# Optimization experiments

Hardware: AMD Instinct MI355X
Metric: run time of the kernel (lower is better)

Reference implementation:

```python
import jax, jax.numpy as jnp
import numpy as np

PRE_NMS_THRESH = 0.05
PRE_NMS_TOP_N = 1000
NMS_THRESH = 0.6
FPN_POST_NMS_TOP_N = 100
MIN_SIZE = 0.0
NUM_CLASSES = 80
BBOX_W = (10.0, 10.0, 5.0, 5.0)
SCALE_CLAMP = float(np.log(1000.0 / 16.0))
CLASS_OFFSET = 2000.0  # > max image coordinate after clipping
N_IMG = 16
LEVELS = [(100, 152, 8, 64), (50, 76, 16, 128), (25, 38, 32, 256), (13, 19, 64, 512), (7, 10, 128, 1024)]


def _make_anchors(H, W, stride, size):
    cx = np.arange(W, dtype=np.float32) * stride
    cy = np.arange(H, dtype=np.float32) * stride
    xx, yy = np.meshgrid(cx, cy)
    ctr = np.stack([xx, yy, xx, yy], -1).reshape(-1, 4)
    base = np.array([-size / 2.0, -size / 2.0, size / 2.0, size / 2.0], np.float32)
    return jnp.asarray((ctr + base).astype(np.float32))


def setup_inputs() -> dict:
    key = jax.random.key(0)
    ks = jax.random.split(key, 10)
    inp = {}
    for i, (H, W, st, sz) in enumerate(LEVELS):
        inp[f"cls{i}"] = jax.random.normal(ks[i], (N_IMG, NUM_CLASSES, H, W), jnp.float32) * 2.0 - 4.0
        inp[f"reg{i}"] = jax.random.normal(ks[5 + i], (N_IMG, 4, H, W), jnp.float32)
        inp[f"anc{i}"] = _make_anchors(H, W, st, sz)
    inp["image_sizes"] = jnp.tile(jnp.array([[800, 1216]], jnp.int32), (N_IMG, 1))
    return inp


def _decode(deltas, anchors):
    wx, wy, ww, wh = BBOX_W
    w = anchors[..., 2] - anchors[..., 0] + 1.0
    h = anchors[..., 3] - anchors[..., 1] + 1.0
    cx = anchors[..., 0] + 0.5 * w
    cy = anchors[..., 1] + 0.5 * h
    dx = deltas[..., 0] / wx
    dy = deltas[..., 1] / wy
    dw = jnp.minimum(deltas[..., 2] / ww, SCALE_CLAMP)
    dh = jnp.minimum(deltas[..., 3] / wh, SCALE_CLAMP)
    pcx = dx * w + cx
    pcy = dy * h + cy
    pw = jnp.exp(dw) * w
    ph = jnp.exp(dh) * h
    return jnp.stack([pcx - 0.5 * (pw - 1.0), pcy - 0.5 * (ph - 1.0),
                      pcx + 0.5 * (pw - 1.0), pcy + 0.5 * (ph - 1.0)], -1)


def _level(cls, reg, anc):
    n, C, H, W = cls.shape  # A = 1
    scores = jax.nn.sigmoid(jnp.transpose(cls, (0, 2, 3, 1)).reshape(n, -1, C))  # [n, HW, C]
    regf = jnp.transpose(reg, (0, 2, 3, 1)).reshape(n, -1, 4)  # [n, HW, 4]
    flat = scores.reshape(n, -1)
    masked = jnp.where(flat > PRE_NMS_THRESH, flat, 0.0)
    vals, idx = jax.lax.top_k(masked, PRE_NMS_TOP_N)  # emulates thresh + per-image clamp
    loc = idx // C
    cl = idx % C
    deltas = jnp.take_along_axis(regf, loc[..., None], axis=1)  # [n, K, 4]
    boxes = _decode(deltas, anc[loc])
    valid = vals > PRE_NMS_THRESH
    sc = jnp.where(valid, jnp.sqrt(jnp.maximum(vals, 1e-12)), 0.0)
    return boxes, sc, cl, valid


def _nms_keep(boxes, classes, valid):
    M = boxes.shape[0]
    b = boxes + classes.astype(boxes.dtype)[:, None] * CLASS_OFFSET  # class-aware offsets
    areas = (b[:, 2] - b[:, 0]) * (b[:, 3] - b[:, 1])
    ar = jnp.arange(M)

    def body(i, sup):
        bi = b[i]
        xx1 = jnp.maximum(bi[0], b[:, 0])
        yy1 = jnp.maximum(bi[1], b[:, 1])
        xx2 = jnp.minimum(bi[2], b[:, 2])
        yy2 = jnp.minimum(bi[3], b[:, 3])
        inter = jnp.maximum(xx2 - xx1, 0.0) * jnp.maximum(yy2 - yy1, 0.0)
        iou = inter / (areas[i] + areas - inter + 1e-9)
        new = sup | ((iou > NMS_THRESH) & (ar > i))
        return jnp.where(sup[i], sup, new)

    sup = jax.lax.fori_loop(0, M, body, ~valid)
    return ~sup


def _forward(cls_l, reg_l, anc_l, image_sizes):
    outs = [_level(c, r, a) for c, r, a in zip(cls_l, reg_l, anc_l)]
    boxes = jnp.concatenate([o[0] for o in outs], 1)   # [N, M, 4]
    scores = jnp.concatenate([o[1] for o in outs], 1)  # [N, M]
    classes = jnp.concatenate([o[2] for o in outs], 1)
    valid = jnp.concatenate([o[3] for o in outs], 1)
    hs = image_sizes[:, 0:1].astype(boxes.dtype)
    ws = image_sizes[:, 1:2].astype(boxes.dtype)
    x1 = jnp.clip(boxes[..., 0], 0.0, ws)
    y1 = jnp.clip(boxes[..., 1], 0.0, hs)
    x2 = jnp.clip(boxes[..., 2], 0.0, ws)
    y2 = jnp.clip(boxes[..., 3], 0.0, hs)
    boxes = jnp.stack([x1, y1, x2, y2], -1)
    nonempty = ((x2 - x1) > MIN_SIZE) & ((y2 - y1) > MIN_SIZE)
    valid = valid & nonempty
    scores = jnp.where(valid, scores, 0.0)
    order = jnp.argsort(-scores, axis=1)
    boxes = jnp.take_along_axis(boxes, order[..., None], 1)
    scores = jnp.take_along_axis(scores, order, 1)
    classes = jnp.take_along_axis(classes, order, 1)
    valid = jnp.take_along_axis(valid, order, 1)
    keep = jax.vmap(_nms_keep)(boxes, classes, valid)
    fs = jnp.where(keep, scores, 0.0)
    top_scores, idx = jax.lax.top_k(fs, FPN_POST_NMS_TOP_N)  # kthvalue filter == top-k
    top_boxes = jnp.take_along_axis(boxes, idx[..., None], 1)
    top_classes = jnp.take_along_axis(classes, idx, 1)
    return top_boxes, top_scores, top_classes


def reference(cls0, cls1, cls2, cls3, cls4, reg0, reg1, reg2, reg3, reg4,
              anc0, anc1, anc2, anc3, anc4, image_sizes):
    return _forward([cls0, cls1, cls2, cls3, cls4],
                    [reg0, reg1, reg2, reg3, reg4],
                    [anc0, anc1, anc2, anc3, anc4], image_sizes)
```

## Files before the change

kernel.cpp:

```cpp
#include <hip/hip_runtime.h>
#include <stdint.h>
#include <math.h>

#define NLEV 5
#define NIMG 16
#define NCLS 80
#define TOPK 1000
#define MTOT 5000
#define LPAD 1024
#define BNDCAP 4096
#define SEGCAP 3072
#define NBINS 288
#define BIN0 7846
#define OUTK 100
#define CHUNK 8192
#define NCHUNK 3216
#define CCAND 1024
#define ROWCAP 8192
#define CCAP 512

__device__ __constant__ int c_HW[NLEV]   = {15200, 3800, 950, 247, 70};
__device__ __constant__ int c_E[NLEV]    = {1216000, 304000, 76000, 19760, 5600};
__device__ __constant__ int c_cpr[NLEV]  = {149, 38, 10, 3, 1};
__device__ __constant__ int c_cbase[NLEV + 1] = {0, 2384, 2992, 3152, 3200, 3216};
__device__ __constant__ int c_GB[NLEV]   = {256, 230, 179, 64, 0};

struct Params {
    const float* cls[NLEV];
    const float* reg[NLEV];
    const float* anc[NLEV];
    const int* imsize;
};

__device__ inline void decode_entry(const Params& P, int img, int lvl, uint32_t idx,
                                    float bclip[4], int* cls_out, bool* nonempty) {
    int HW = c_HW[lvl];
    int loc = (int)idx / NCLS;
    int c = (int)idx - loc * NCLS;
    const float* a = P.anc[lvl] + 4 * loc;
    float a0 = a[0], a1 = a[1], a2 = a[2], a3 = a[3];
    const float* rg = P.reg[lvl] + (size_t)img * 4 * HW + loc;
    float d0 = rg[0], d1 = rg[HW], d2 = rg[2 * HW], d3 = rg[3 * HW];
    float w = a2 - a0 + 1.0f, h = a3 - a1 + 1.0f;
    float cx = a0 + 0.5f * w, cy = a1 + 0.5f * h;
    float dx = d0 / 10.0f, dy = d1 / 10.0f;
    const float SCALE_CLAMP = 4.135166556742356f;
    float dw = fminf(d2 / 5.0f, SCALE_CLAMP);
    float dh = fminf(d3 / 5.0f, SCALE_CLAMP);
    float pcx = dx * w + cx, pcy = dy * h + cy;
    float pw = (float)exp((double)dw) * w;
    float ph = (float)exp((double)dh) * h;
    float x1 = pcx - 0.5f * (pw - 1.0f), y1 = pcy - 0.5f * (ph - 1.0f);
    float x2 = pcx + 0.5f * (pw - 1.0f), y2 = pcy + 0.5f * (ph - 1.0f);
    float Hs = (float)P.imsize[img * 2 + 0];
    float Ws = (float)P.imsize[img * 2 + 1];
    float x1c = fminf(fmaxf(x1, 0.0f), Ws);
    float y1c = fminf(fmaxf(y1, 0.0f), Hs);
    float x2c = fminf(fmaxf(x2, 0.0f), Ws);
    float y2c = fminf(fmaxf(y2, 0.0f), Hs);
    bclip[0] = x1c; bclip[1] = y1c; bclip[2] = x2c; bclip[3] = y2c;
    *cls_out = c;
    *nonempty = ((x2c - x1c) > 0.0f) && ((y2c - y1c) > 0.0f);
}

__device__ inline float sigmoid_f(float x) {
    return (float)(1.0 / (1.0 + exp(-(double)x)));
}

__device__ inline uint32_t f2o(float f) {
    uint32_t b = __float_as_uint(f);
    return (b & 0x80000000u) ? ~b : (b | 0x80000000u);
}
__device__ inline float o2f(uint32_t o) {
    uint32_t b = (o & 0x80000000u) ? (o & 0x7FFFFFFFu) : ~o;
    return __uint_as_float(b);
}

__device__ inline void chunk_map(int bid, int* lvl, int* img, int* start, int* end) {
    int l = 0;
#pragma unroll
    for (int q = 1; q < NLEV; q++) if (bid >= c_cbase[q]) l = q;
    int r = bid - c_cbase[l];
    int cpr = c_cpr[l];
    int im = r / cpr;
    int ch = r - im * cpr;
    int E = c_E[l];
    int st = ch * CHUNK;
    *lvl = l; *img = im; *start = st; *end = min(st + CHUNK, E);
}

__global__ __launch_bounds__(320) void k_thr(float* T, uint32_t* hist, uint32_t* cnts) {
    int b = blockIdx.x;
    int t = threadIdx.x;
    if (t < NBINS) hist[b * NBINS + t] = 0;
    if (b == 1 && t < 240) cnts[t] = 0;
    if (b == 0 && t < NBINS) {
        uint32_t lo = f2o(-4.0f), hi = f2o(20.0f);
        while (hi - lo > 1u) {
            uint32_t mid = lo + ((hi - lo) >> 1);
            float xm = o2f(mid);
            float s = sigmoid_f(xm);
            bool pass = (s > 0.05f) && (((int)(__float_as_uint(s) >> 17) - BIN0) >= t);
            if (pass) hi = mid; else lo = mid;
        }
        float xr = o2f(hi);
        float sv = sigmoid_f(xr);
        bool ok = (sv > 0.05f) && (((int)(__float_as_uint(sv) >> 17) - BIN0) >= t);
        T[t] = ok ? xr : __uint_as_float(0x7F800000u);
    }
}

__global__ __launch_bounds__(256) void k_hist(Params P, const float* __restrict__ T,
                                              uint32_t* __restrict__ hist,
                                              uint16_t* __restrict__ segMax16,
                                              uint64_t* __restrict__ rowCand,
                                              uint32_t* __restrict__ rowCnt,
                                              uint32_t* __restrict__ fbflag,
                                              uint32_t* __restrict__ histBad) {
    __shared__ uint32_t lh[NBINS];
    __shared__ float sT[NBINS];
    __shared__ uint64_t cand[CCAND];
    __shared__ uint32_t ccnt, wbase;
    int l, img, start, end;
    chunk_map(blockIdx.x, &l, &img, &start, &end);
    for (int b = threadIdx.x; b < NBINS; b += 256) { lh[b] = 0; sT[b] = T[b]; }
    if (threadIdx.x == 0) ccnt = 0;
    __syncthreads();
    float gthr = sT[c_GB[l]];
    int HW = c_HW[l];
    int row = l * NIMG + img;
    const float4* __restrict__ p = (const float4*)(P.cls[l] + (size_t)img * c_E[l] + start);
    int n4 = (end - start) >> 2;
    float4 r[8];
#pragma unroll
    for (int u = 0; u < 8; u++) {
        int f = u * 256 + threadIdx.x;
        r[u] = (f < n4) ? p[f] : make_float4(-1e30f, -1e30f, -1e30f, -1e30f);
    }
#pragma unroll
    for (int u = 0; u < 8; u++) {
        float4 x4 = r[u];
        float m4 = fmaxf(fmaxf(x4.x, x4.y), fmaxf(x4.z, x4.w));
        float sm = m4;
        sm = fmaxf(sm, __shfl_xor(sm, 1));
        sm = fmaxf(sm, __shfl_xor(sm, 2));
        sm = fmaxf(sm, __shfl_xor(sm, 4));
        if ((threadIdx.x & 7) == 0) {
            int s = u * 32 + (threadIdx.x >> 3);
            uint32_t mb = __float_as_uint(sm);
            uint16_t ub = (sm >= 0.0f) ? (uint16_t)((mb + 0xFFFFu) >> 16) : (uint16_t)(mb >> 16);
            segMax16[(size_t)blockIdx.x * 256 + s] = ub;
        }
        float xs[4] = {x4.x, x4.y, x4.z, x4.w};
#pragma unroll
        for (int k = 0; k < 4; k++) {
            float xv = xs[k];
            if (xv >= gthr) {
                uint32_t lp = atomicAdd(&ccnt, 1u);
                if (lp < CCAND) {
                    uint32_t pos = (uint32_t)((u * 256 + threadIdx.x) * 4 + k);
                    cand[lp] = ((uint64_t)__float_as_uint(xv) << 32) | pos;
                }
            }
        }
    }
    __syncthreads();
    uint32_t cc = ccnt;
    uint32_t n = min(cc, (uint32_t)CCAND);
    if (threadIdx.x == 0) {
        wbase = atomicAdd(&rowCnt[row], n);
        if (cc > CCAND) { atomicOr(&fbflag[row], 1u); atomicOr(&histBad[row], 1u); }
        else if (wbase + n > ROWCAP) atomicOr(&fbflag[row], 1u);
    }
    __syncthreads();
    for (uint32_t i = threadIdx.x; i < n; i += 256) {
        uint64_t rec = cand[i];
        float xv = __uint_as_float((uint32_t)(rec >> 32));
        int pos = (int)(rec & 0xFFFFu);
        float se = 1.0f / (1.0f + __expf(-xv));
        int b = (int)(__float_as_uint(se) >> 17) - BIN0;
        b = min(max(b, 0), NBINS - 1);
        while (b > 0 && xv < sT[b]) b--;
        while (b + 1 < NBINS && xv >= sT[b + 1]) b++;
        atomicAdd(&lh[b], 1u);
        int q2 = start + pos;
        int c = q2 / HW;
        int pidx = q2 - c * HW;
        uint32_t idx = (uint32_t)(pidx * NCLS + c);
        uint32_t gpos = wbase + i;
        if (gpos < ROWCAP)
            rowCand[(size_t)row * ROWCAP + gpos] = ((uint64_t)__float_as_uint(xv) << 32) | idx;
    }
    __syncthreads();
    for (int b = threadIdx.x; b < NBINS; b += 256) {
        uint32_t c = lh[b];
        if (c) atomicAdd(&hist[row * NBINS + b], c);
    }
}

__global__ __launch_bounds__(320) void k_scan(const uint32_t* hist, int* sel,
                                              uint32_t* fbflag, const uint32_t* histBad) {
    __shared__ uint32_t lh[NBINS];
    int row = blockIdx.x;
    if (threadIdx.x < NBINS) lh[threadIdx.x] = hist[row * NBINS + threadIdx.x];
    __syncthreads();
    if (threadIdx.x == 0) {
        int l = row / NIMG;
        int GBl = c_GB[l];
        int cum = 0, B = -3, need = 0, cab = 0;
        if (histBad[row] == 0) {
            for (int b = NBINS - 1; b >= GBl; b--) {
                int c = (int)lh[b];
                if (cum + c >= TOPK) { B = b; cab = cum; need = TOPK - cum; break; }
                cum += c;
            }
        }
        if (B == -3) {
            sel[row * 4 + 0] = -2;
            sel[row * 4 + 1] = 0; sel[row * 4 + 2] = 0; sel[row * 4 + 3] = 0;
            fbflag[row] = 1;
        } else {
            sel[row * 4 + 0] = B;
            sel[row * 4 + 1] = cab;
            sel[row * 4 + 2] = need;
            sel[row * 4 + 3] = cum;
        }
    }
}

__global__ __launch_bounds__(1024) void k_fb(Params P, const float* T,
                                             const uint16_t* segMax16, int* sel) {
    int row = blockIdx.x;
    if (sel[row * 4 + 0] != -2) return;
    __shared__ uint32_t lh[NBINS];
    int lvl = row / NIMG, img = row - lvl * NIMG;
    int E = c_E[lvl];
    int segbase = (c_cbase[lvl] + img * c_cpr[lvl]) * 256;
    int nsr = c_cpr[lvl] * 256;
    float t0 = T[0];
    for (int b = threadIdx.x; b < NBINS; b += 1024) lh[b] = 0;
    __syncthreads();
    const float4* p4 = (const float4*)(P.cls[lvl] + (size_t)img * E);
    for (int s = threadIdx.x; s < nsr; s += 1024) {
        uint16_t ub = segMax16[segbase + s];
        if (__uint_as_float((uint32_t)ub << 16) >= t0) {
            for (int f = 0; f < 8; f++) {
                int e0 = s * 32 + f * 4;
                if (e0 >= E) break;
                float4 x4 = p4[s * 8 + f];
                float xs[4] = {x4.x, x4.y, x4.z, x4.w};
#pragma unroll
                for (int k = 0; k < 4; k++) {
                    float xv = xs[k];
                    if (xv >= t0) {
                        float sc = sigmoid_f(xv);
                        int b = (int)(__float_as_uint(sc) >> 17) - BIN0;
                        b = min(max(b, 0), NBINS - 1);
                        atomicAdd(&lh[b], 1u);
                    }
                }
            }
        }
    }
    __syncthreads();
    if (threadIdx.x == 0) {
        int cum = 0, B = -1, need = 0, cab = 0;
        for (int b = NBINS - 1; b >= 0; b--) {
            int c = (int)lh[b];
            if (cum + c >= TOPK) { B = b; cab = cum; need = TOPK - cum; break; }
            cum += c;
        }
        if (B < 0) { cab = cum; need = 0; }
        sel[row * 4 + 0] = B;
        sel[row * 4 + 1] = cab;
        sel[row * 4 + 2] = need;
        sel[row * 4 + 3] = cum;
    }
}

__global__ __launch_bounds__(1024) void k_selkr(Params P, const int* sel, const float* T,
                                                const uint16_t* segMax16,
                                                const uint64_t* rowCand, const uint32_t* rowCnt,
                                                const uint32_t* fbflag, uint64_t* keys) {
    __shared__ uint32_t segs[SEGCAP];
    __shared__ uint64_t smain[1024];
    __shared__ uint64_t sbnd[BNDCAP];
    __shared__ uint64_t kk[LPAD];
    __shared__ uint32_t cnt0, cnt1, nseg;
    int blk = blockIdx.x;
    int img = blk / NLEV, lvl = blk - img * NLEV;
    int row = lvl * NIMG + img;
    int B = sel[row * 4 + 0], cab = sel[row * 4 + 1];
    int need = sel[row * 4 + 2], cum = sel[row * 4 + 3];
    float xt = T[max(B, 0)];
    float tB1 = T[min(B + 1, NBINS - 1)];
    int HW = c_HW[lvl];
    int E = c_E[lvl];
    if (threadIdx.x == 0) { cnt0 = 0; cnt1 = 0; nseg = 0; }
    __syncthreads();
    uint32_t rcnt = rowCnt[row];
    bool fb = (fbflag[row] != 0) || (rcnt > ROWCAP);
    if (!fb) {
        const uint64_t* rc = rowCand + (size_t)row * ROWCAP;
        int cntr = (int)rcnt;
        for (int i = threadIdx.x; i < cntr; i += 1024) {
            uint64_t rec = rc[i];
            float x = __uint_as_float((uint32_t)(rec >> 32));
            if (x >= tB1) {
                uint32_t lp = atomicAdd(&cnt0, 1u);
                if (lp < 1024) smain[lp] = rec;
            } else if (x >= xt) {
                uint32_t lp = atomicAdd(&cnt1, 1u);
                if (lp < BNDCAP) sbnd[lp] = rec;
            }
        }
    } else {
        int segbase = (c_cbase[lvl] + img * c_cpr[lvl]) * 256;
        int nsr = c_cpr[lvl] * 256;
        for (int s = threadIdx.x; s < nsr; s += 1024) {
            uint16_t ub = segMax16[segbase + s];
            if (__uint_as_float((uint32_t)ub << 16) >= xt) {
                uint32_t q = atomicAdd(&nseg, 1u);
                if (q < SEGCAP) segs[q] = (uint32_t)s;
            }
        }
        __syncthreads();
        uint32_t ns = nseg;
        const float4* p4 = (const float4*)(P.cls[lvl] + (size_t)img * E);
        if (ns <= SEGCAP) {
            for (uint32_t wk = threadIdx.x; wk < ns * 8; wk += 1024) {
                int s = (int)segs[wk >> 3];
                int fo = (int)(wk & 7);
                int e0 = s * 32 + fo * 4;
                if (e0 >= E) continue;
                float4 x4 = p4[s * 8 + fo];
                float xs[4] = {x4.x, x4.y, x4.z, x4.w};
#pragma unroll
                for (int k = 0; k < 4; k++) {
                    float xv = xs[k];
                    if (xv >= xt) {
                        int q2 = e0 + k;
                        int c = q2 / HW;
                        int pidx = q2 - c * HW;
                        uint32_t idx = (uint32_t)(pidx * NCLS + c);
                        uint64_t rec = ((uint64_t)__float_as_uint(xv) << 32) | idx;
                        if (xv >= tB1) {
                            uint32_t lp = atomicAdd(&cnt0, 1u);
                            if (lp < 1024) smain[lp] = rec;
                        } else {
                            uint32_t lp = atomicAdd(&cnt1, 1u);
                            if (lp < BNDCAP) sbnd[lp] = rec;
                        }
                    }
                }
            }
        } else {
            for (int s = threadIdx.x; s < nsr; s += 1024) {
                uint16_t ub = segMax16[segbase + s];
                if (__uint_as_float((uint32_t)ub << 16) >= xt) {
                    for (int f = 0; f < 8; f++) {
                        int e0 = s * 32 + f * 4;
                        if (e0 >= E) break;
                        float4 x4 = p4[s * 8 + f];
                        float xs[4] = {x4.x, x4.y, x4.z, x4.w};
#pragma unroll
                        for (int k = 0; k < 4; k++) {
                            float xv = xs[k];
                            if (xv >= xt) {
                                int q2 = e0 + k;
                                int c = q2 / HW;
                                int pidx = q2 - c * HW;
                                uint32_t idx = (uint32_t)(pidx * NCLS + c);
                                uint64_t rec = ((uint64_t)__float_as_uint(xv) << 32) | idx;
                                if (xv >= tB1) {
                                    uint32_t lp = atomicAdd(&cnt0, 1u);
                                    if (lp < 1024) smain[lp] = rec;
                                } else {
                                    uint32_t lp = atomicAdd(&cnt1, 1u);
                                    if (lp < BNDCAP) sbnd[lp] = rec;
                                }
                            }
                        }
                    }
                }
            }
        }
    }
    __syncthreads();
    int take = 0;
    int cnt = min((int)cnt1, BNDCAP);
    if (need > 0) {
        for (int i = threadIdx.x; i < cnt; i += 1024) {
            uint64_t r = sbnd[i];
            float x = __uint_as_float((uint32_t)(r >> 32));
            uint32_t sb = __float_as_uint(sigmoid_f(x));
            sbnd[i] = ((uint64_t)(uint32_t)(~sb) << 32) | (uint32_t)r;
        }
        __syncthreads();
        int N = 64; while (N < cnt) N <<= 1;
        for (int i = threadIdx.x; i < N; i += 1024) {
            if (i >= cnt) sbnd[i] = ~0ULL;
        }
        __syncthreads();
        for (int k = 2; k <= N; k <<= 1) {
            for (int j = k >> 1; j > 0; j >>= 1) {
                for (int i = threadIdx.x; i < N; i += 1024) {
                    int ixj = i ^ j;
                    if (ixj > i) {
                        uint64_t A = sbnd[i], Bv = sbnd[ixj];
                        bool up = ((i & k) == 0);
                        if (up ? (A > Bv) : (A < Bv)) { sbnd[i] = Bv; sbnd[ixj] = A; }
                    }
                }
                __syncthreads();
            }
        }
        take = min(need, cnt);
    }
    int nmain = min((int)cnt0, 1024);
    int filled = (B < 0) ? cum : (cab + take);
    for (int slot = threadIdx.x; slot < LPAD; slot += 1024) {
        uint64_t key;
        if (slot >= TOPK) key = ~0ULL;
        else {
            uint32_t bits = 0, idx = 0;
            if (slot < filled) {
                if (slot < cab || B < 0) {
                    if (slot < nmain) {
                        uint64_t r = smain[slot];
                        float x = __uint_as_float((uint32_t)(r >> 32));
                        bits = __float_as_uint(sigmoid_f(x));
                        idx = (uint32_t)r;
                    }
                } else {
                    uint64_t wv = sbnd[slot - cab];
                    bits = ~((uint32_t)(wv >> 32));
                    idx = (uint32_t)wv;
                }
            }
            uint32_t be = 0;
            if (bits != 0) {
                float bc[4]; int cc; bool ne;
                decode_entry(P, img, lvl, idx, bc, &cc, &ne);
                if (ne) be = bits;
            }
            key = ((uint64_t)(uint32_t)(~be) << 24) | ((uint64_t)lvl << 21) | (uint64_t)idx;
        }
        kk[slot] = key;
    }
    __syncthreads();
    for (int k = 2; k <= LPAD; k <<= 1) {
        for (int j = k >> 1; j > 0; j >>= 1) {
            for (int i = threadIdx.x; i < LPAD; i += 1024) {
                int ixj = i ^ j;
                if (ixj > i) {
                    uint64_t A = kk[i], Bv = kk[ixj];
                    bool up = ((i & k) == 0);
                    if (up ? (A > Bv) : (A < Bv)) { kk[i] = Bv; kk[ixj] = A; }
                }
            }
            __syncthreads();
        }
    }
    uint64_t* g = keys + (size_t)blk * LPAD;
    for (int i = threadIdx.x; i < LPAD; i += 1024) g[i] = kk[i];
}

__global__ __launch_bounds__(1024) void k_merge(Params P, const uint64_t* keys,
                                                float4* boff, float* area, float4* bclip,
                                                float* scs, int* clss,
                                                uint8_t* keepB, uint8_t* clsB) {
    __shared__ uint64_t sl[NLEV * LPAD];
    int img = blockIdx.x >> 2;
    int part = blockIdx.x & 3;
    const uint64_t* g = keys + (size_t)img * NLEV * LPAD;
    for (int i = threadIdx.x; i < NLEV * LPAD; i += 1024) sl[i] = g[i];
    __syncthreads();
    const int gb = img * MTOT;
    int e0 = part * (NLEV * LPAD / 4);
    int e1 = e0 + (NLEV * LPAD / 4);
    for (int e = e0 + threadIdx.x; e < e1; e += 1024) {
        int l = e >> 10, i = e & (LPAD - 1);
        if (i >= TOPK) continue;
        uint64_t K = sl[e];
        int rank = i;
#pragma unroll
        for (int l2 = 0; l2 < NLEV; l2++) {
            if (l2 == l) continue;
            const uint64_t* s2 = &sl[l2 << 10];
            int lo = 0, hi = TOPK;
            while (lo < hi) {
                int mid = (lo + hi) >> 1;
                if (s2[mid] < K) lo = mid + 1; else hi = mid;
            }
            rank += lo;
        }
        uint32_t bits = ~((uint32_t)(K >> 24));
        int lvl = (int)((K >> 21) & 7);
        uint32_t idx = (uint32_t)(K & 0x1FFFFF);
        float bc[4]; int cc; bool ne;
        decode_entry(P, img, lvl, idx, bc, &cc, &ne);
        float sc = 0.0f;
        if (bits != 0) {
            float s = __uint_as_float(bits);
            sc = sqrtf(fmaxf(s, 1e-12f));
        }
        float off = (float)cc * 2000.0f;
        float b0 = bc[0] + off, b1 = bc[1] + off, b2 = bc[2] + off, b3 = bc[3] + off;
        int t = gb + rank;
        boff[t] = make_float4(b0, b1, b2, b3);
        area[t] = (b2 - b0) * (b3 - b1);
        bclip[t] = make_float4(bc[0], bc[1], bc[2], bc[3]);
        scs[t] = sc;
        clss[t] = cc;
        keepB[t] = 0;
        clsB[t] = (sc != 0.0f) ? (uint8_t)cc : (uint8_t)0xFF;
    }
}

__global__ __launch_bounds__(64) void k_cnms(const float4* boff, const float* area,
                                             const uint8_t* clsB, uint8_t* keepB) {
    __shared__ float sx1[CCAP], sy1[CCAP], sx2[CCAP], sy2[CCAP], sar[CCAP];
    __shared__ uint16_t ranks[CCAP];
    int img = blockIdx.x / NCLS;
    int cls = blockIdx.x - img * NCLS;
    int lane = threadIdx.x;
    const int gb = img * MTOT;

    int n = 0;
    const uchar4* cp = (const uchar4*)(clsB + gb);
    for (int base = 0; base < 1250; base += 64) {
        int q = base + lane;
        uchar4 cv = (q < 1250) ? cp[q] : make_uchar4(255, 255, 255, 255);
#pragma unroll
        for (int b = 0; b < 4; b++) {
            int cb = (b == 0) ? cv.x : (b == 1) ? cv.y : (b == 2) ? cv.z : cv.w;
            bool pred = (cb == cls);
            uint64_t mask = __ballot(pred);
            int pos = n + (int)__popcll(mask & ((1ULL << lane) - 1ULL));
            if (pred && pos < CCAP) ranks[pos] = (uint16_t)(q * 4 + b);
            n += (int)__popcll(mask);
        }
    }
    n = min(n, CCAP);
    __syncthreads();
    if (n == 0) return;

    for (int i = lane; i < n; i += 64) {
        int t = ranks[i];
        float4 b = boff[gb + t];
        sx1[i] = b.x; sy1[i] = b.y; sx2[i] = b.z; sy2[i] = b.w;
        sar[i] = area[gb + t];
    }
    __syncthreads();

    uint64_t m[CCAP / 64];
#pragma unroll
    for (int c = 0; c < CCAP / 64; c++) m[c] = 0ULL;
#pragma unroll
    for (int c = 0; c < CCAP / 64; c++) {
        if (c * 64 >= n) break;
        for (int ii = 0; ii < 64; ii++) {
            int i = c * 64 + ii;
            if (i >= n) break;
            if ((m[c] >> ii) & 1ULL) continue;
            float bx1 = sx1[i], by1 = sy1[i], bx2 = sx2[i], by2 = sy2[i], bai = sar[i];
            if (lane == 0) keepB[gb + ranks[i]] = 1;
#pragma unroll
            for (int c2 = 0; c2 < CCAP / 64; c2++) {
                if (c2 < c) continue;
                if (c2 * 64 >= n) break;
                int j = c2 * 64 + lane;
                float xx1 = fmaxf(bx1, sx1[j]), yy1 = fmaxf(by1, sy1[j]);
                float xx2 = fminf(bx2, sx2[j]), yy2 = fminf(by2, sy2[j]);
                float inter = fmaxf(xx2 - xx1, 0.0f) * fmaxf(yy2 - yy1, 0.0f);
                float iou = inter / (bai + sar[j] - inter + 1e-9f);
                bool pr = (j > i) && (j < n) && (iou > 0.6f);
                m[c2] |= __ballot(pr);
            }
        }
    }
}

__global__ __launch_bounds__(64) void k_out(const float4* bclip, const float* scs,
                                            const int* clss, const uint8_t* keepB, float* out) {
    __shared__ int keptIdx[OUTK];
    int img = blockIdx.x;
    int lane = threadIdx.x;
    const int gb = img * MTOT;
    int kc = 0;
    for (int base = 0; base < MTOT && kc < OUTK; base += 64) {
        int t = base + lane;
        bool pred = (t < MTOT) && (keepB[gb + t] != 0);
        uint64_t mask = __ballot(pred);
        int pos = kc + (int)__popcll(mask & ((1ULL << lane) - 1ULL));
        if (pred && pos < OUTK) keptIdx[pos] = t;
        kc = min(kc + (int)__popcll(mask), OUTK);
    }
    for (int base = 0; base < MTOT && kc < OUTK; base += 64) {
        int t = base + lane;
        bool pred = (t < MTOT) && (keepB[gb + t] == 0);
        uint64_t mask = __ballot(pred);
        int pos = kc + (int)__popcll(mask & ((1ULL << lane) - 1ULL));
        if (pred && pos < OUTK) keptIdx[pos] = t | (1 << 30);
        kc = min(kc + (int)__popcll(mask), OUTK);
    }
    __syncthreads();
    for (int t = lane; t < OUTK; t += 64) {
        int ke = keptIdx[t];
        bool fil = (ke >> 30) & 1;
        int e = ke & 0x3FFFFFFF;
        float4 b = bclip[gb + e];
        out[((size_t)img * OUTK + t) * 4 + 0] = b.x;
        out[((size_t)img * OUTK + t) * 4 + 1] = b.y;
        out[((size_t)img * OUTK + t) * 4 + 2] = b.z;
        out[((size_t)img * OUTK + t) * 4 + 3] = b.w;
        out[NIMG * OUTK * 4 + img * OUTK + t] = fil ? 0.0f : scs[gb + e];
        out[NIMG * OUTK * 4 + NIMG * OUTK + img * OUTK + t] = (float)clss[gb + e];
    }
}

extern "C" void kernel_launch(void* const* d_in, const int* in_sizes, int n_in,
                              void* d_out, int out_size, void* d_ws, size_t ws_size,
                              hipStream_t stream) {
    Params P;
    for (int l = 0; l < 5; l++) {
        P.cls[l] = (const float*)d_in[l * 3 + 0];
        P.reg[l] = (const float*)d_in[l * 3 + 1];
        P.anc[l] = (const float*)d_in[l * 3 + 2];
    }
    P.imsize = (const int*)d_in[15];

    char* w = (char*)d_ws;
    uint64_t* rowCand  = (uint64_t*)(w + 0);
    float4*   boff     = (float4*)(w + 0);
    float*    area     = (float*)(w + 1280000);
    float4*   bclipb   = (float4*)(w + 1600000);
    float*    scs      = (float*)(w + 2880000);
    int*      clss     = (int*)(w + 3200000);
    int*      sel      = (int*)(w + 5242880);
    float*    T        = (float*)(w + 5244160);
    uint32_t* hist     = (uint32_t*)(w + 5245312);
    uint32_t* rowCnt   = (uint32_t*)(w + 5337472);
    uint32_t* fbflag   = (uint32_t*)(w + 5337792);
    uint32_t* histBad  = (uint32_t*)(w + 5338112);
    uint64_t* keys     = (uint64_t*)(w + 5338432);
    uint8_t*  keepB    = (uint8_t*)(w + 5993792);
    uint8_t*  clsB     = (uint8_t*)(w + 6073792);
    uint16_t* segMax16 = (uint16_t*)(w + 6153792);

    k_thr<<<80, 320, 0, stream>>>(T, hist, rowCnt);
    k_hist<<<NCHUNK, 256, 0, stream>>>(P, T, hist, segMax16, rowCand, rowCnt, fbflag, histBad);
    k_scan<<<80, 320, 0, stream>>>(hist, sel, fbflag, histBad);
    k_fb<<<80, 1024, 0, stream>>>(P, T, segMax16, sel);
    k_selkr<<<NIMG * NLEV, 1024, 0, stream>>>(P, sel, T, segMax16, rowCand, rowCnt, fbflag, keys);
    k_merge<<<NIMG * 4, 1024, 0, stream>>>(P, keys, boff, area, bclipb, scs, clss, keepB, clsB);
    k_cnms<<<NIMG * NCLS, 64, 0, stream>>>(boff, area, clsB, keepB);
    k_out<<<NIMG, 64, 0, stream>>>(bclipb, scs, clss, keepB, (float*)d_out);
}
```

Measured before the change: 177.7 us.

## Drop segment-max index and merge scan with fallback histogram kernel

Removes the per-32-element segment max computation and its stores from the histogram kernel. The rarely taken fallback paths now scan the full class-logit row directly instead of skipping segments by their max. The scan and fallback-histogram kernels are fused into one launch, saving a kernel launch and the segMax16 writes. The cost is that any row that falls back must read its whole row with scalar loads, which is slow if fallback ever triggers.

```diff
diff --git a/kernel.cpp b/kernel.cpp
--- a/kernel.cpp
+++ b/kernel.cpp
@@ -9,7 +9,6 @@
 #define MTOT 5000
 #define LPAD 1024
 #define BNDCAP 4096
-#define SEGCAP 3072
 #define NBINS 288
 #define BIN0 7846
 #define OUTK 100
@@ -112,7 +111,6 @@
 
 __global__ __launch_bounds__(256) void k_hist(Params P, const float* __restrict__ T,
                                               uint32_t* __restrict__ hist,
-                                              uint16_t* __restrict__ segMax16,
                                               uint64_t* __restrict__ rowCand,
                                               uint32_t* __restrict__ rowCnt,
                                               uint32_t* __restrict__ fbflag,
@@ -140,17 +138,6 @@
 #pragma unroll
     for (int u = 0; u < 8; u++) {
         float4 x4 = r[u];
-        float m4 = fmaxf(fmaxf(x4.x, x4.y), fmaxf(x4.z, x4.w));
-        float sm = m4;
-        sm = fmaxf(sm, __shfl_xor(sm, 1));
-        sm = fmaxf(sm, __shfl_xor(sm, 2));
-        sm = fmaxf(sm, __shfl_xor(sm, 4));
-        if ((threadIdx.x & 7) == 0) {
-            int s = u * 32 + (threadIdx.x >> 3);
-            uint32_t mb = __float_as_uint(sm);
-            uint16_t ub = (sm >= 0.0f) ? (uint16_t)((mb + 0xFFFFu) >> 16) : (uint16_t)(mb >> 16);
-            segMax16[(size_t)blockIdx.x * 256 + s] = ub;
-        }
         float xs[4] = {x4.x, x4.y, x4.z, x4.w};
 #pragma unroll
         for (int k = 0; k < 4; k++) {
@@ -198,14 +185,17 @@
     }
 }
 
-__global__ __launch_bounds__(320) void k_scan(const uint32_t* hist, int* sel,
-                                              uint32_t* fbflag, const uint32_t* histBad) {
+__global__ __launch_bounds__(1024) void k_scanfb(Params P, const float* T,
+                                                 const uint32_t* hist, int* sel,
+                                                 uint32_t* fbflag, const uint32_t* histBad) {
     __shared__ uint32_t lh[NBINS];
+    __shared__ int s_bad;
     int row = blockIdx.x;
     if (threadIdx.x < NBINS) lh[threadIdx.x] = hist[row * NBINS + threadIdx.x];
-    __syncthreads();
+    if (threadIdx.x == 0) s_bad = 0;
+    __syncthreads();
+    int l = row / NIMG;
     if (threadIdx.x == 0) {
-        int l = row / NIMG;
         int GBl = c_GB[l];
         int cum = 0, B = -3, need = 0, cab = 0;
         if (histBad[row] == 0) {
@@ -216,8 +206,7 @@
             }
         }
         if (B == -3) {
-            sel[row * 4 + 0] = -2;
-            sel[row * 4 + 1] = 0; sel[row * 4 + 2] = 0; sel[row * 4 + 3] = 0;
+            s_bad = 1;
             fbflag[row] = 1;
         } else {
             sel[row * 4 + 0] = B;
@@ -226,40 +215,21 @@
             sel[row * 4 + 3] = cum;
         }
     }
-}
-
-__global__ __launch_bounds__(1024) void k_fb(Params P, const float* T,
-                                             const uint16_t* segMax16, int* sel) {
-    int row = blockIdx.x;
-    if (sel[row * 4 + 0] != -2) return;
-    __shared__ uint32_t lh[NBINS];
-    int lvl = row / NIMG, img = row - lvl * NIMG;
-    int E = c_E[lvl];
-    int segbase = (c_cbase[lvl] + img * c_cpr[lvl]) * 256;
-    int nsr = c_cpr[lvl] * 256;
+    __syncthreads();
+    if (!s_bad) return;
+    int img = row - l * NIMG;
+    int E = c_E[l];
     float t0 = T[0];
     for (int b = threadIdx.x; b < NBINS; b += 1024) lh[b] = 0;
     __syncthreads();
-    const float4* p4 = (const float4*)(P.cls[lvl] + (size_t)img * E);
-    for (int s = threadIdx.x; s < nsr; s += 1024) {
-        uint16_t ub = segMax16[segbase + s];
-        if (__uint_as_float((uint32_t)ub << 16) >= t0) {
-            for (int f = 0; f < 8; f++) {
-                int e0 = s * 32 + f * 4;
-                if (e0 >= E) break;
-                float4 x4 = p4[s * 8 + f];
-                float xs[4] = {x4.x, x4.y, x4.z, x4.w};
-#pragma unroll
-                for (int k = 0; k < 4; k++) {
-                    float xv = xs[k];
-                    if (xv >= t0) {
-                        float sc = sigmoid_f(xv);
-                        int b = (int)(__float_as_uint(sc) >> 17) - BIN0;
-                        b = min(max(b, 0), NBINS - 1);
-                        atomicAdd(&lh[b], 1u);
-                    }
-                }
-            }
+    const float* base = P.cls[l] + (size_t)img * E;
+    for (int e = threadIdx.x; e < E; e += 1024) {
+        float xv = base[e];
+        if (xv >= t0) {
+            float sc = sigmoid_f(xv);
+            int b = (int)(__float_as_uint(sc) >> 17) - BIN0;
+            b = min(max(b, 0), NBINS - 1);
+            atomicAdd(&lh[b], 1u);
         }
     }
     __syncthreads();
@@ -279,14 +249,12 @@
 }
 
 __global__ __launch_bounds__(1024) void k_selkr(Params P, const int* sel, const float* T,
-                                                const uint16_t* segMax16,
                                                 const uint64_t* rowCand, const uint32_t* rowCnt,
                                                 const uint32_t* fbflag, uint64_t* keys) {
-    __shared__ uint32_t segs[SEGCAP];
     __shared__ uint64_t smain[1024];
     __shared__ uint64_t sbnd[BNDCAP];
     __shared__ uint64_t kk[LPAD];
-    __shared__ uint32_t cnt0, cnt1, nseg;
+    __shared__ uint32_t cnt0, cnt1;
     int blk = blockIdx.x;
     int img = blk / NLEV, lvl = blk - img * NLEV;
     int row = lvl * NIMG + img;
@@ -296,7 +264,7 @@
     float tB1 = T[min(B + 1, NBINS - 1)];
     int HW = c_HW[lvl];
     int E = c_E[lvl];
-    if (threadIdx.x == 0) { cnt0 = 0; cnt1 = 0; nseg = 0; }
+    if (threadIdx.x == 0) { cnt0 = 0; cnt1 = 0; }
     __syncthreads();
     uint32_t rcnt = rowCnt[row];
     bool fb = (fbflag[row] != 0) || (rcnt > ROWCAP);
@@ -315,73 +283,20 @@
             }
         }
     } else {
-        int segbase = (c_cbase[lvl] + img * c_cpr[lvl]) * 256;
-        int nsr = c_cpr[lvl] * 256;
-        for (int s = threadIdx.x; s < nsr; s += 1024) {
-            uint16_t ub = segMax16[segbase + s];
-            if (__uint_as_float((uint32_t)ub << 16) >= xt) {
-                uint32_t q = atomicAdd(&nseg, 1u);
-                if (q < SEGCAP) segs[q] = (uint32_t)s;
-            }
-        }
-        __syncthreads();
-        uint32_t ns = nseg;
-        const float4* p4 = (const float4*)(P.cls[lvl] + (size_t)img * E);
-        if (ns <= SEGCAP) {
-            for (uint32_t wk = threadIdx.x; wk < ns * 8; wk += 1024) {
-                int s = (int)segs[wk >> 3];
-                int fo = (int)(wk & 7);
-                int e0 = s * 32 + fo * 4;
-                if (e0 >= E) continue;
-                float4 x4 = p4[s * 8 + fo];
-                float xs[4] = {x4.x, x4.y, x4.z, x4.w};
-#pragma unroll
-                for (int k = 0; k < 4; k++) {
-                    float xv = xs[k];
-                    if (xv >= xt) {
-                        int q2 = e0 + k;
-                        int c = q2 / HW;
-                        int pidx = q2 - c * HW;
-                        uint32_t idx = (uint32_t)(pidx * NCLS + c);
-                        uint64_t rec = ((uint64_t)__float_as_uint(xv) << 32) | idx;
-                        if (xv >= tB1) {
-                            uint32_t lp = atomicAdd(&cnt0, 1u);
-                            if (lp < 1024) smain[lp] = rec;
-                        } else {
-                            uint32_t lp = atomicAdd(&cnt1, 1u);
-                            if (lp < BNDCAP) sbnd[lp] = rec;
-                        }
-                    }
-                }
-            }
-        } else {
-            for (int s = threadIdx.x; s < nsr; s += 1024) {
-                uint16_t ub = segMax16[segbase + s];
-                if (__uint_as_float((uint32_t)ub << 16) >= xt) {
-                    for (int f = 0; f < 8; f++) {
-                        int e0 = s * 32 + f * 4;
-                        if (e0 >= E) break;
-                        float4 x4 = p4[s * 8 + f];
-                        float xs[4] = {x4.x, x4.y, x4.z, x4.w};
-#pragma unroll
-                        for (int k = 0; k < 4; k++) {
-                            float xv = xs[k];
-                            if (xv >= xt) {
-                                int q2 = e0 + k;
-                                int c = q2 / HW;
-                                int pidx = q2 - c * HW;
-                                uint32_t idx = (uint32_t)(pidx * NCLS + c);
-                                uint64_t rec = ((uint64_t)__float_as_uint(xv) << 32) | idx;
-                                if (xv >= tB1) {
-                                    uint32_t lp = atomicAdd(&cnt0, 1u);
-                                    if (lp < 1024) smain[lp] = rec;
-                                } else {
-                                    uint32_t lp = atomicAdd(&cnt1, 1u);
-                                    if (lp < BNDCAP) sbnd[lp] = rec;
-                                }
-                            }
-                        }
-                    }
+        const float* base = P.cls[lvl] + (size_t)img * E;
+        for (int e = threadIdx.x; e < E; e += 1024) {
+            float xv = base[e];
+            if (xv >= xt) {
+                int c = e / HW;
+                int pidx = e - c * HW;
+                uint32_t idx = (uint32_t)(pidx * NCLS + c);
+                uint64_t rec = ((uint64_t)__float_as_uint(xv) << 32) | idx;
+                if (xv >= tB1) {
+                    uint32_t lp = atomicAdd(&cnt0, 1u);
+                    if (lp < 1024) smain[lp] = rec;
+                } else {
+                    uint32_t lp = atomicAdd(&cnt1, 1u);
+                    if (lp < BNDCAP) sbnd[lp] = rec;
                 }
             }
         }
@@ -647,13 +562,11 @@
     uint64_t* keys     = (uint64_t*)(w + 5338432);
     uint8_t*  keepB    = (uint8_t*)(w + 5993792);
     uint8_t*  clsB     = (uint8_t*)(w + 6073792);
-    uint16_t* segMax16 = (uint16_t*)(w + 6153792);
 
     k_thr<<<80, 320, 0, stream>>>(T, hist, rowCnt);
-    k_hist<<<NCHUNK, 256, 0, stream>>>(P, T, hist, segMax16, rowCand, rowCnt, fbflag, histBad);
-    k_scan<<<80, 320, 0, stream>>>(hist, sel, fbflag, histBad);
-    k_fb<<<80, 1024, 0, stream>>>(P, T, segMax16, sel);
-    k_selkr<<<NIMG * NLEV, 1024, 0, stream>>>(P, sel, T, segMax16, rowCand, rowCnt, fbflag, keys);
+    k_hist<<<NCHUNK, 256, 0, stream>>>(P, T, hist, rowCand, rowCnt, fbflag, histBad);
+    k_scanfb<<<80, 1024, 0, stream>>>(P, T, hist, sel, fbflag, histBad);
+    k_selkr<<<NIMG * NLEV, 1024, 0, stream>>>(P, sel, T, rowCand, rowCnt, fbflag, keys);
     k_merge<<<NIMG * 4, 1024, 0, stream>>>(P, keys, boff, area, bclipb, scs, clss, keepB, clsB);
     k_cnms<<<NIMG * NCLS, 64, 0, stream>>>(boff, area, clsB, keepB);
     k_out<<<NIMG, 64, 0, stream>>>(bclipb, scs, clss, keepB, (float*)d_out);
```

Result: faster. 169.0 us (-4.9%).
